# Kernel tuning notes

Measured on AMD Instinct MI355X. Metric: run time of the kernel, lower is better.

The kernel has to match this reference:

```python
import jax, jax.numpy as jnp
import numpy as np

B, N, D, HID, NB, NC = 64, 256, 1024, 512, 2, 1000
EPS = 1e-5

def _ln(x, g, b):
    m = x.mean(-1, keepdims=True)
    v = ((x - m) ** 2).mean(-1, keepdims=True)
    return (x - m) / jnp.sqrt(v + EPS) * g + b

def _gelu(x):
    return jax.nn.gelu(x, approximate=False)

def _knn_adjacency(x, k):
    # x: [N, D] -> symmetric-normalized kNN adjacency with self loops, [N, N]
    n = x.shape[0]
    sq = jnp.sum(x * x, axis=-1)
    d2 = sq[:, None] + sq[None, :] - 2.0 * (x @ x.T)
    d2 = jnp.where(jnp.eye(n, dtype=bool), jnp.inf, d2)  # exclude self from kNN
    idx = jax.lax.top_k(-d2, k)[1]                       # [N, k] nearest neighbors
    A = jnp.zeros((n, n), x.dtype).at[jnp.arange(n)[:, None], idx].set(1.0)
    A = jnp.maximum(A, A.T) + jnp.eye(n, dtype=x.dtype)  # symmetrize + self loops
    dinv = jax.lax.rsqrt(A.sum(-1))                      # D^{-1/2}
    return A * dinv[:, None] * dinv[None, :]

def setup_inputs() -> dict:
    key = jax.random.key(0)
    ks = jax.random.split(key, 8)
    s = lambda i, shape: jax.random.normal(ks[i], shape, jnp.float32) * 0.02
    return {
        "tokens": jax.random.normal(ks[0], (B, N, D), jnp.float32),
        "W1": s(1, (NB, D, HID)), "b1": jnp.zeros((NB, HID), jnp.float32),
        "W2": s(2, (NB, HID, D)), "b2": jnp.zeros((NB, D), jnp.float32),
        "g1": jnp.ones((NB, D), jnp.float32), "be1": jnp.zeros((NB, D), jnp.float32),
        "g2": jnp.ones((NB, D), jnp.float32), "be2": jnp.zeros((NB, D), jnp.float32),
        "gr": jnp.ones((D,), jnp.float32), "br": jnp.zeros((D,), jnp.float32),
        "Wc": s(3, (D, NC)), "bc": jnp.zeros((NC,), jnp.float32),
        "k": 8,
    }

def reference(tokens, W1, b1, W2, b2, g1, be1, g2, be2, gr, br, Wc, bc, k):
    # tokens: [B, N, D] backbone features flattened to nodes (eval mode: dropout = identity)
    A = jax.vmap(lambda t: _knn_adjacency(t, k))(tokens)  # [B, N, N]
    x = tokens
    for i in range(NB):  # GraphBlock
        h = _ln(x, g1[i], be1[i])
        h = _gelu(jnp.einsum("bij,bjh->bih", A, h @ W1[i] + b1[i]))  # A_hat @ lin1
        h = jnp.einsum("bij,bjd->bid", A, h @ W2[i] + b2[i])          # A_hat @ lin2
        x = x + h
        x = x + _gelu(_ln(x, g2[i], be2[i]))
    x = _gelu(_ln(x, gr, br))      # readout
    out = x.mean(axis=1)           # graph mean-pool, [B, D]
    return out @ Wc + bc           # logits [B, NC]
```

## Files before the change

### kernel.cpp

```cpp
#include <hip/hip_runtime.h>
#include <hip/hip_bf16.h>
#include <math.h>

constexpr int Bb  = 64;
constexpr int Nn_ = 256;
constexpr int Dd  = 1024;
constexpr int Hh  = 512;
constexpr int NC  = 1000;
constexpr float LN_EPS = 1e-5f;

#define DEV __device__ __forceinline__

typedef unsigned short u16;
typedef __attribute__((ext_vector_type(8))) short bf16x8;
typedef __attribute__((ext_vector_type(4))) float f32x4;
typedef __attribute__((ext_vector_type(4))) unsigned short u16x4;

DEV float gelu_f(float x) { return 0.5f * x * (1.0f + erff(x * 0.70710678118654752f)); }
DEV u16 bfb(float x) { __hip_bfloat16 h = __float2bfloat16(x); u16 u; __builtin_memcpy(&u, &h, 2); return u; }
DEV float fromb(u16 u) { unsigned int w = (unsigned int)u << 16; float f; __builtin_memcpy(&f, &w, 4); return f; }

DEV void gload16(const void* g, void* l) {
    __builtin_amdgcn_global_load_lds(
        (const __attribute__((address_space(1))) void*)(uintptr_t)g,
        (__attribute__((address_space(3))) void*)(uintptr_t)l, 16, 0, 0);
}

enum { EP_BIAS_BF_CT = 0, EP_GELU_BF_CT = 1, EP_BF = 2, EP_SBIAS_ADD_F32 = 3 };

template<int EPI>
__global__ __launch_bounds__(256) void mgemm_k(
    const u16* __restrict__ Ag, const u16* __restrict__ Bg, void* __restrict__ Cg,
    const float* __restrict__ bias, const float* __restrict__ addsrc, const float* __restrict__ rsA,
    int M, int Nc, int K, long sA, long sB, long sC)
{
    __shared__ __align__(16) u16 sm[2][2][128 * 32];
    const int tid = threadIdx.x;
    const int l = tid & 63, w = tid >> 6;
    const int wm = w >> 1, wn = w & 1;
    const int bm = blockIdx.y * 128, bn = blockIdx.x * 128;
    const int z = blockIdx.z;
    const u16* Ab  = Ag + (long)z * sA;
    const u16* Bbp = Bg + (long)z * sB;

    f32x4 acc[4][4] = {};
    const int nt = K >> 5;

    auto stage = [&](int db, int t) {
        const long kk = (long)t << 5;
        #pragma unroll
        for (int i = 0; i < 2; ++i) {
            const int o = w * 1024 + i * 4096 + l * 16;
            const int r = o >> 6;
            const int g = ((o >> 4) & 3) ^ ((r >> 1) & 3);
            gload16(Ab  + (long)(bm + r) * K + kk + g * 8, (char*)&sm[db][0][0] + o);
            gload16(Bbp + (long)(bn + r) * K + kk + g * 8, (char*)&sm[db][1][0] + o);
        }
    };

    stage(0, 0);
    __syncthreads();
    for (int t = 0; t < nt; ++t) {
        const int db = t & 1;
        if (t + 1 < nt) stage(db ^ 1, t + 1);
        const int lr = l & 15, g = l >> 4;
        bf16x8 af[4], bfr[4];
        #pragma unroll
        for (int fm = 0; fm < 4; ++fm) {
            const int r = wm * 64 + fm * 16 + lr;
            af[fm] = *(const bf16x8*)((const char*)&sm[db][0][0] + r * 64 + ((g ^ ((r >> 1) & 3)) << 4));
        }
        #pragma unroll
        for (int fn = 0; fn < 4; ++fn) {
            const int r = wn * 64 + fn * 16 + lr;
            bfr[fn] = *(const bf16x8*)((const char*)&sm[db][1][0] + r * 64 + ((g ^ ((r >> 1) & 3)) << 4));
        }
        #pragma unroll
        for (int fm = 0; fm < 4; ++fm)
            #pragma unroll
            for (int fn = 0; fn < 4; ++fn)
                acc[fm][fn] = __builtin_amdgcn_mfma_f32_16x16x32_bf16(af[fm], bfr[fn], acc[fm][fn], 0, 0, 0);
        __syncthreads();
    }

    const int lr = l & 15, lg = l >> 4;
    if constexpr (EPI == EP_SBIAS_ADD_F32) {
        float* Cb = (float*)Cg;
        #pragma unroll
        for (int fm = 0; fm < 4; ++fm)
            #pragma unroll
            for (int fn = 0; fn < 4; ++fn) {
                const int gc = bn + wn * 64 + fn * 16 + lr;
                const float bv = bias[gc];
                #pragma unroll
                for (int rg = 0; rg < 4; ++rg) {
                    const int gm = bm + wm * 64 + fm * 16 + lg * 4 + rg;
                    Cb[(long)gm * Nc + gc] = acc[fm][fn][rg] + rsA[gm] * bv + addsrc[(long)gm * Nc + gc];
                }
            }
    } else if constexpr (EPI == EP_BIAS_BF_CT || EPI == EP_GELU_BF_CT) {
        #pragma unroll
        for (int fm = 0; fm < 4; ++fm) {
            const int gm0 = bm + wm * 64 + fm * 16 + lg * 4;
            #pragma unroll
            for (int fn = 0; fn < 4; ++fn) {
                const int gc = bn + wn * 64 + fn * 16 + lr;
                u16x4 vals;
                if constexpr (EPI == EP_BIAS_BF_CT) {
                    const float bv = bias[gc];
                    #pragma unroll
                    for (int rg = 0; rg < 4; ++rg) vals[rg] = bfb(acc[fm][fn][rg] + bv);
                } else {
                    #pragma unroll
                    for (int rg = 0; rg < 4; ++rg) vals[rg] = bfb(gelu_f(acc[fm][fn][rg]));
                }
                long addr;
                if constexpr (EPI == EP_BIAS_BF_CT)
                    addr = (long)(gm0 >> 8) * ((long)Nc * 256) + (long)gc * 256 + (gm0 & 255);
                else
                    addr = (long)z * sC + (long)gc * 256 + gm0;
                *(u16x4*)&((u16*)Cg)[addr] = vals;
            }
        }
    } else {
        u16* Cb = (u16*)Cg + (long)z * sC;
        #pragma unroll
        for (int fm = 0; fm < 4; ++fm)
            #pragma unroll
            for (int fn = 0; fn < 4; ++fn)
                #pragma unroll
                for (int rg = 0; rg < 4; ++rg) {
                    const int gm = bm + wm * 64 + fm * 16 + lg * 4 + rg;
                    const int gc = bn + wn * 64 + fn * 16 + lr;
                    Cb[(long)gm * Nc + gc] = bfb(acc[fm][fn][rg]);
                }
    }
}

__global__ __launch_bounds__(256) void d2mm_k(
    const u16* __restrict__ HL, const float* __restrict__ sq, float* __restrict__ d2)
{
    __shared__ __align__(16) u16 sm[2][4][128 * 32];
    const int tid = threadIdx.x;
    const int l = tid & 63, w = tid >> 6;
    const int wm = w >> 1, wn = w & 1;

    const int lid = blockIdx.x;
    const int xcd = lid & 7, q = lid >> 3;
    const int j   = q % 3;
    const int z   = (q / 3) * 8 + xcd;
    const int bm  = (j == 2) ? 128 : 0;
    const int bn  = (j == 0) ? 0 : 128;

    const u16* Hb = HL + (long)z * Nn_ * 2048;

    f32x4 acc[4][4] = {};

    auto stage = [&](int db, int t) {
        const long kk = (long)t << 5;
        #pragma unroll
        for (int i = 0; i < 2; ++i) {
            const int o = w * 1024 + i * 4096 + l * 16;
            const int r = o >> 6;
            const int g = ((o >> 4) & 3) ^ ((r >> 1) & 3);
            const long ka = kk + g * 8;
            gload16(Hb + (long)(bm + r) * 2048 + ka,        (char*)&sm[db][0][0] + o);
            gload16(Hb + (long)(bm + r) * 2048 + 1024 + ka, (char*)&sm[db][1][0] + o);
            gload16(Hb + (long)(bn + r) * 2048 + ka,        (char*)&sm[db][2][0] + o);
            gload16(Hb + (long)(bn + r) * 2048 + 1024 + ka, (char*)&sm[db][3][0] + o);
        }
    };

    stage(0, 0);
    __syncthreads();
    for (int t = 0; t < 32; ++t) {
        const int db = t & 1;
        if (t + 1 < 32) stage(db ^ 1, t + 1);
        const int lr = l & 15, g = l >> 4;
        bf16x8 ah[4], al[4], bh[4], bl[4];
        #pragma unroll
        for (int fm = 0; fm < 4; ++fm) {
            const int r = wm * 64 + fm * 16 + lr;
            const int off = r * 64 + ((g ^ ((r >> 1) & 3)) << 4);
            ah[fm] = *(const bf16x8*)((const char*)&sm[db][0][0] + off);
            al[fm] = *(const bf16x8*)((const char*)&sm[db][1][0] + off);
        }
        #pragma unroll
        for (int fn = 0; fn < 4; ++fn) {
            const int r = wn * 64 + fn * 16 + lr;
            const int off = r * 64 + ((g ^ ((r >> 1) & 3)) << 4);
            bh[fn] = *(const bf16x8*)((const char*)&sm[db][2][0] + off);
            bl[fn] = *(const bf16x8*)((const char*)&sm[db][3][0] + off);
        }
        #pragma unroll
        for (int fm = 0; fm < 4; ++fm)
            #pragma unroll
            for (int fn = 0; fn < 4; ++fn) {
                acc[fm][fn] = __builtin_amdgcn_mfma_f32_16x16x32_bf16(ah[fm], bh[fn], acc[fm][fn], 0, 0, 0);
                acc[fm][fn] = __builtin_amdgcn_mfma_f32_16x16x32_bf16(ah[fm], bl[fn], acc[fm][fn], 0, 0, 0);
                acc[fm][fn] = __builtin_amdgcn_mfma_f32_16x16x32_bf16(al[fm], bh[fn], acc[fm][fn], 0, 0, 0);
            }
        __syncthreads();
    }

    const int lr = l & 15, lg = l >> 4;
    const float* sqb = sq + z * Nn_;
    float* ob = d2 + (long)z * Nn_ * Nn_;
    #pragma unroll
    for (int fm = 0; fm < 4; ++fm)
        #pragma unroll
        for (int fn = 0; fn < 4; ++fn)
            #pragma unroll
            for (int rg = 0; rg < 4; ++rg) {
                const int gm = bm + wm * 64 + fm * 16 + lg * 4 + rg;
                const int gc = bn + wn * 64 + fn * 16 + lr;
                float v = sqb[gm] + sqb[gc] - 2.0f * acc[fm][fn][rg];
                if (gm == gc) v = INFINITY;
                ob[(long)gm * Nn_ + gc] = v;
                if (j == 1) ob[(long)gc * Nn_ + gm] = v;
            }
}

__global__ __launch_bounds__(256) void prep_k(const float* __restrict__ in, u16* __restrict__ hilo,
    float* __restrict__ sq, u16* __restrict__ lnout,
    const float* __restrict__ g, const float* __restrict__ bvec)
{
    const long row = blockIdx.x;
    const int t = threadIdx.x;
    const float4 v = *(const float4*)&in[row * Dd + t * 4];
    float xs[4] = {v.x, v.y, v.z, v.w};

    u16x4 hi, lo;
    #pragma unroll
    for (int j = 0; j < 4; ++j) {
        hi[j] = bfb(xs[j]);
        lo[j] = bfb(xs[j] - fromb(hi[j]));
    }
    *(u16x4*)&hilo[row * 2048 + t * 4]        = hi;
    *(u16x4*)&hilo[row * 2048 + 1024 + t * 4] = lo;

    float s  = xs[0] + xs[1] + xs[2] + xs[3];
    float s2 = xs[0]*xs[0] + xs[1]*xs[1] + xs[2]*xs[2] + xs[3]*xs[3];
    #pragma unroll
    for (int o = 32; o > 0; o >>= 1) { s += __shfl_down(s, o); s2 += __shfl_down(s2, o); }
    __shared__ float sh[8];
    const int wid = t >> 6, lane = t & 63;
    if (lane == 0) { sh[wid] = s; sh[4 + wid] = s2; }
    __syncthreads();
    const float S  = sh[0] + sh[1] + sh[2] + sh[3];
    const float S2 = sh[4] + sh[5] + sh[6] + sh[7];
    if (t == 0) sq[row] = S2;
    const float mean = S * (1.0f / Dd);
    const float rstd = rsqrtf(S2 * (1.0f / Dd) - mean * mean + LN_EPS);
    const float4 gv = *(const float4*)&g[t * 4];
    const float4 bv = *(const float4*)&bvec[t * 4];
    const float gs[4] = {gv.x, gv.y, gv.z, gv.w};
    const float bs[4] = {bv.x, bv.y, bv.z, bv.w};
    u16x4 ov;
    #pragma unroll
    for (int j = 0; j < 4; ++j) ov[j] = bfb((xs[j] - mean) * rstd * gs[j] + bs[j]);
    *(u16x4*)&lnout[row * Dd + t * 4] = ov;
}

__global__ __launch_bounds__(256) void transw_k(const float* __restrict__ in, u16* __restrict__ out,
                                                int R, int C, long sIn, long sOut)
{
    __shared__ u16 t[32][33];
    const int z = blockIdx.z;
    const float* ib = in + (long)z * sIn;
    u16* ob = out + (long)z * sOut;
    const int r0 = blockIdx.y * 32, c0 = blockIdx.x * 32;
    const int tr = threadIdx.x >> 3, tc4 = (threadIdx.x & 7) * 4;
    const float* p = ib + (long)(r0 + tr) * C + c0 + tc4;
    #pragma unroll
    for (int j = 0; j < 4; ++j) t[tr][tc4 + j] = bfb(p[j]);
    __syncthreads();
    u16* q = ob + (long)(c0 + tr) * R + r0 + tc4;
    #pragma unroll
    for (int j = 0; j < 4; ++j) q[j] = t[tc4 + j][tr];
}

__global__ __launch_bounds__(256) void transc_k(const float* __restrict__ Wc, float* __restrict__ WcT)
{
    __shared__ float t[32][33];
    const int r0 = blockIdx.y * 32, c0 = blockIdx.x * 32;
    const int tr = threadIdx.x >> 3, tc4 = (threadIdx.x & 7) * 4;
    #pragma unroll
    for (int j = 0; j < 4; ++j) {
        const int c = c0 + tc4 + j;
        t[tr][tc4 + j] = (c < NC) ? Wc[(long)(r0 + tr) * NC + c] : 0.f;
    }
    __syncthreads();
    const int oc = c0 + tr;
    if (oc < NC) {
        #pragma unroll
        for (int j = 0; j < 4; ++j)
            WcT[(long)oc * Dd + r0 + tc4 + j] = t[tc4 + j][tr];
    }
}

template<int LAST>
__global__ __launch_bounds__(256) void ln2f_k(const float* __restrict__ xin,
    float* __restrict__ xout, u16* __restrict__ lnout,
    const float* __restrict__ g2, const float* __restrict__ be2,
    const float* __restrict__ gn, const float* __restrict__ bn)
{
    const long row = blockIdx.x;
    const int t = threadIdx.x;
    const int wid = t >> 6, lane = t & 63;
    __shared__ float sh[8];

    float4 v = *(const float4*)&xin[row * Dd + t * 4];
    float xs[4] = {v.x, v.y, v.z, v.w};
    float s = xs[0] + xs[1] + xs[2] + xs[3];
    float s2 = xs[0]*xs[0] + xs[1]*xs[1] + xs[2]*xs[2] + xs[3]*xs[3];
    #pragma unroll
    for (int o = 32; o > 0; o >>= 1) { s += __shfl_down(s, o); s2 += __shfl_down(s2, o); }
    if (lane == 0) { sh[wid] = s; sh[4 + wid] = s2; }
    __syncthreads();
    {
        const float S = sh[0] + sh[1] + sh[2] + sh[3];
        const float S2 = sh[4] + sh[5] + sh[6] + sh[7];
        const float mean = S * (1.0f / Dd);
        const float rstd = rsqrtf(S2 * (1.0f / Dd) - mean * mean + LN_EPS);
        const float4 gv = *(const float4*)&g2[t * 4];
        const float4 bv = *(const float4*)&be2[t * 4];
        const float gs[4] = {gv.x, gv.y, gv.z, gv.w};
        const float bs[4] = {bv.x, bv.y, bv.z, bv.w};
        #pragma unroll
        for (int j = 0; j < 4; ++j)
            xs[j] = xs[j] + gelu_f((xs[j] - mean) * rstd * gs[j] + bs[j]);
    }
    __syncthreads();
    float t1 = xs[0] + xs[1] + xs[2] + xs[3];
    float t2 = xs[0]*xs[0] + xs[1]*xs[1] + xs[2]*xs[2] + xs[3]*xs[3];
    #pragma unroll
    for (int o = 32; o > 0; o >>= 1) { t1 += __shfl_down(t1, o); t2 += __shfl_down(t2, o); }
    if (lane == 0) { sh[wid] = t1; sh[4 + wid] = t2; }
    __syncthreads();
    const float S = sh[0] + sh[1] + sh[2] + sh[3];
    const float S2 = sh[4] + sh[5] + sh[6] + sh[7];
    const float mean = S * (1.0f / Dd);
    const float rstd = rsqrtf(S2 * (1.0f / Dd) - mean * mean + LN_EPS);
    const float4 gv = *(const float4*)&gn[t * 4];
    const float4 bv = *(const float4*)&bn[t * 4];
    const float gs[4] = {gv.x, gv.y, gv.z, gv.w};
    const float bs[4] = {bv.x, bv.y, bv.z, bv.w};
    u16x4 ov;
    if constexpr (LAST) {
        #pragma unroll
        for (int j = 0; j < 4; ++j) ov[j] = bfb(gelu_f((xs[j] - mean) * rstd * gs[j] + bs[j]));
    } else {
        *(float4*)&xout[row * Dd + t * 4] = make_float4(xs[0], xs[1], xs[2], xs[3]);
        #pragma unroll
        for (int j = 0; j < 4; ++j) ov[j] = bfb((xs[j] - mean) * rstd * gs[j] + bs[j]);
    }
    *(u16x4*)&lnout[row * Dd + t * 4] = ov;
}

__global__ __launch_bounds__(256) void topk_k(const float* __restrict__ d2, float* __restrict__ Aout,
                                              const int* __restrict__ kptr)
{
    const int k = *kptr;
    const int wid = threadIdx.x >> 6, lane = threadIdx.x & 63;
    const long row = (long)blockIdx.x * 4 + wid;
    const long b = row >> 8;
    const int  i = (int)(row & 255);
    const float* dr = d2 + row * Nn_;
    float v[4];
    bool sel[4] = {false, false, false, false};
    #pragma unroll
    for (int c = 0; c < 4; ++c) v[c] = dr[lane + 64 * c];
    for (int it = 0; it < k; ++it) {
        float bv = INFINITY; int bi = 1 << 20;
        #pragma unroll
        for (int c = 0; c < 4; ++c) {
            const int idx = lane + 64 * c;
            if (!sel[c] && (v[c] < bv || (v[c] == bv && idx < bi))) { bv = v[c]; bi = idx; }
        }
        #pragma unroll
        for (int o = 32; o > 0; o >>= 1) {
            float ov = __shfl_xor(bv, o); int oi = __shfl_xor(bi, o);
            if (ov < bv || (ov == bv && oi < bi)) { bv = ov; bi = oi; }
        }
        #pragma unroll
        for (int c = 0; c < 4; ++c) if (lane + 64 * c == bi) sel[c] = true;
        if (lane == 0) {
            Aout[(b * Nn_ + i) * Nn_ + bi] = 1.0f;
            Aout[(b * Nn_ + bi) * Nn_ + i] = 1.0f;
        }
    }
    if (lane == 0) Aout[(b * Nn_ + i) * Nn_ + i] = 1.0f;
}

__global__ __launch_bounds__(256) void deg_k(const float* __restrict__ A, float* __restrict__ dinv)
{
    const int wid = threadIdx.x >> 6, lane = threadIdx.x & 63;
    const long row = (long)blockIdx.x * 4 + wid;
    const float* ar = A + row * Nn_;
    float s = 0.f;
    #pragma unroll
    for (int c = 0; c < 4; ++c) s += ar[lane + 64 * c];
    #pragma unroll
    for (int o = 32; o > 0; o >>= 1) s += __shfl_down(s, o);
    if (lane == 0) dinv[row] = rsqrtf(s);
}

__global__ __launch_bounds__(256) void scalebf2_k(const float* __restrict__ A, const float* __restrict__ dinv,
                                                  u16* __restrict__ out, float* __restrict__ rsA)
{
    const int wid = threadIdx.x >> 6, lane = threadIdx.x & 63;
    const long row = (long)blockIdx.x * 4 + wid;
    const long b = row >> 8;
    const float di = dinv[row];
    const int j0 = lane * 4;
    const float4 dj = *(const float4*)&dinv[b * Nn_ + j0];
    const float4 a = *(const float4*)&A[row * Nn_ + j0];
    const float v0 = a.x * di * dj.x, v1 = a.y * di * dj.y, v2 = a.z * di * dj.z, v3 = a.w * di * dj.w;
    u16x4 o = { bfb(v0), bfb(v1), bfb(v2), bfb(v3) };
    *(u16x4*)&out[row * Nn_ + j0] = o;
    float s = v0 + v1 + v2 + v3;
    #pragma unroll
    for (int off = 32; off > 0; off >>= 1) s += __shfl_down(s, off);
    if (lane == 0) rsA[row] = s;
}

__global__ __launch_bounds__(256) void poolb_k(const u16* __restrict__ y, float* __restrict__ pooled)
{
    const int d = blockIdx.x * 256 + threadIdx.x;
    const int b = blockIdx.y;
    const u16* yb = y + (long)b * Nn_ * Dd + d;
    float s = 0.f;
    #pragma unroll 4
    for (int n = 0; n < Nn_; ++n) s += fromb(yb[(long)n * Dd]);
    pooled[b * Dd + d] = s * (1.0f / Nn_);
}

__global__ __launch_bounds__(256) void cls2_k(const float* __restrict__ pooled, const float* __restrict__ WcT,
    const float* __restrict__ bc, float* __restrict__ out)
{
    const int w = threadIdx.x >> 6, lane = threadIdx.x & 63;
    const int c = blockIdx.x * 4 + w;
    const int b = blockIdx.y;
    const float* wr = WcT + (long)c * Dd;
    const float* p  = pooled + (long)b * Dd;
    float s = 0.f;
    #pragma unroll
    for (int it = 0; it < 4; ++it) {
        const float4 wv = *(const float4*)&wr[it * 256 + lane * 4];
        const float4 pv = *(const float4*)&p[it * 256 + lane * 4];
        s += wv.x * pv.x + wv.y * pv.y + wv.z * pv.z + wv.w * pv.w;
    }
    #pragma unroll
    for (int o = 32; o > 0; o >>= 1) s += __shfl_down(s, o);
    if (lane == 0) out[(long)b * NC + c] = s + bc[c];
}

extern "C" void kernel_launch(void* const* d_in, const int* in_sizes, int n_in,
                              void* d_out, int out_size, void* d_ws, size_t ws_size,
                              hipStream_t stream)
{
    const float* tokens = (const float*)d_in[0];
    const float* W1  = (const float*)d_in[1];
    const float* b1  = (const float*)d_in[2];
    const float* W2  = (const float*)d_in[3];
    const float* b2  = (const float*)d_in[4];
    const float* g1  = (const float*)d_in[5];
    const float* be1 = (const float*)d_in[6];
    const float* g2  = (const float*)d_in[7];
    const float* be2 = (const float*)d_in[8];
    const float* gr  = (const float*)d_in[9];
    const float* br  = (const float*)d_in[10];
    const float* Wc  = (const float*)d_in[11];
    const float* bc  = (const float*)d_in[12];
    const int*   kptr = (const int*)d_in[13];

    constexpr long SZ_XD = (long)Bb * Nn_ * Dd;
    constexpr long SZ_A  = (long)Bb * Nn_ * Nn_;

    char* wp = (char*)d_ws;
    float* x      = (float*)wp; wp += SZ_XD * 4;
    u16*   bufA   = (u16*)wp;   wp += SZ_XD * 2;
    u16*   bufB   = (u16*)wp;   wp += SZ_XD * 2;
    u16*   bufC   = (u16*)wp;   wp += SZ_XD * 2;
    u16*   AmatBF = (u16*)wp;   wp += SZ_A * 2;
    u16*   W1t    = (u16*)wp;   wp += 2L * Dd * Hh * 2;
    u16*   W2t    = (u16*)wp;   wp += 2L * Hh * Dd * 2;
    float* WcT    = (float*)wp; wp += (long)NC * Dd * 4;
    float* sq     = (float*)wp; wp += (long)Bb * Nn_ * 4;
    float* dinv   = (float*)wp; wp += (long)Bb * Nn_ * 4;
    float* rsA    = (float*)wp; wp += (long)Bb * Nn_ * 4;
    float* pooled = (float*)wp; wp += (long)Bb * Dd * 4;

    u16*   hilo  = bufA;
    float* d2f   = x;
    float* AmatF = x + SZ_A;
    u16*   robuf = bufA;

    const dim3 blk(256);

    prep_k<<<Bb * Nn_, blk, 0, stream>>>(tokens, hilo, sq, bufC, g1, be1);

    d2mm_k<<<192, blk, 0, stream>>>(hilo, sq, d2f);
    hipMemsetAsync(AmatF, 0, SZ_A * sizeof(float), stream);
    topk_k<<<Bb * Nn_ / 4, blk, 0, stream>>>(d2f, AmatF, kptr);
    deg_k<<<Bb * Nn_ / 4, blk, 0, stream>>>(AmatF, dinv);
    scalebf2_k<<<Bb * Nn_ / 4, blk, 0, stream>>>(AmatF, dinv, AmatBF, rsA);

    transw_k<<<dim3(Hh / 32, Dd / 32, 2), blk, 0, stream>>>(W1, W1t, Dd, Hh, (long)Dd * Hh, (long)Hh * Dd);
    transw_k<<<dim3(Dd / 32, Hh / 32, 2), blk, 0, stream>>>(W2, W2t, Hh, Dd, (long)Hh * Dd, (long)Dd * Hh);
    transc_k<<<dim3(32, Dd / 32), blk, 0, stream>>>(Wc, WcT);

    for (int i = 0; i < 2; ++i) {
        const float* xin = (i == 0) ? tokens : x;
        mgemm_k<EP_BIAS_BF_CT><<<dim3(Hh / 128, Bb * Nn_ / 128, 1), blk, 0, stream>>>(
            bufC, W1t + (long)i * Hh * Dd, bufB, b1 + i * Hh, nullptr, nullptr,
            Bb * Nn_, Hh, Dd, 0, 0, 0);
        mgemm_k<EP_GELU_BF_CT><<<dim3(Hh / 128, Nn_ / 128, Bb), blk, 0, stream>>>(
            AmatBF, bufB, bufA, nullptr, nullptr, nullptr,
            Nn_, Hh, Nn_, (long)Nn_ * Nn_, (long)Hh * Nn_, (long)Hh * Nn_);
        mgemm_k<EP_BF><<<dim3(Hh / 128, Nn_ / 128, Bb), blk, 0, stream>>>(
            AmatBF, bufA, bufB, nullptr, nullptr, nullptr,
            Nn_, Hh, Nn_, (long)Nn_ * Nn_, (long)Hh * Nn_, (long)Nn_ * Hh);
        mgemm_k<EP_SBIAS_ADD_F32><<<dim3(Dd / 128, Bb * Nn_ / 128, 1), blk, 0, stream>>>(
            bufB, W2t + (long)i * Dd * Hh, x, b2 + i * Dd, xin, rsA,
            Bb * Nn_, Dd, Hh, 0, 0, 0);
        if (i == 0)
            ln2f_k<0><<<Bb * Nn_, blk, 0, stream>>>(x, x, bufC, g2, be2, g1 + Dd, be1 + Dd);
        else
            ln2f_k<1><<<Bb * Nn_, blk, 0, stream>>>(x, nullptr, robuf, g2 + Dd, be2 + Dd, gr, br);
    }

    poolb_k<<<dim3(Dd / 256, Bb), blk, 0, stream>>>(robuf, pooled);
    cls2_k<<<dim3(NC / 4, Bb), blk, 0, stream>>>(pooled, WcT, bc, (float*)d_out);
}
```

Baseline: 429.7 us.

## Move residual add into LN kernel and store residual stream in bf16

The lin2 GEMM epilogue no longer reads the fp32 residual and writes fp32 x. It now writes only a bf16 h buffer. The LN2 kernel reads h plus the residual (fp32 tokens in block 0, bf16 x in block 1), does the add, and stores the updated residual as bf16. This cuts the GEMM epilogue's global traffic and halves the size of the residual buffer, at the cost of lower precision for the residual stream between blocks.

```diff
diff --git a/kernel.cpp b/kernel.cpp
--- a/kernel.cpp
+++ b/kernel.cpp
@@ -26,12 +26,12 @@
         (__attribute__((address_space(3))) void*)(uintptr_t)l, 16, 0, 0);
 }
 
-enum { EP_BIAS_BF_CT = 0, EP_GELU_BF_CT = 1, EP_BF = 2, EP_SBIAS_ADD_F32 = 3 };
+enum { EP_BIAS_BF_CT = 0, EP_GELU_BF_CT = 1, EP_BF = 2, EP_SBIAS_BF = 3 };
 
 template<int EPI>
 __global__ __launch_bounds__(256) void mgemm_k(
     const u16* __restrict__ Ag, const u16* __restrict__ Bg, void* __restrict__ Cg,
-    const float* __restrict__ bias, const float* __restrict__ addsrc, const float* __restrict__ rsA,
+    const float* __restrict__ bias, const float* __restrict__ rsA,
     int M, int Nc, int K, long sA, long sB, long sC)
 {
     __shared__ __align__(16) u16 sm[2][2][128 * 32];
@@ -84,8 +84,8 @@
     }
 
     const int lr = l & 15, lg = l >> 4;
-    if constexpr (EPI == EP_SBIAS_ADD_F32) {
-        float* Cb = (float*)Cg;
+    if constexpr (EPI == EP_SBIAS_BF) {
+        u16* Cb = (u16*)Cg;
         #pragma unroll
         for (int fm = 0; fm < 4; ++fm)
             #pragma unroll
@@ -95,7 +95,7 @@
                 #pragma unroll
                 for (int rg = 0; rg < 4; ++rg) {
                     const int gm = bm + wm * 64 + fm * 16 + lg * 4 + rg;
-                    Cb[(long)gm * Nc + gc] = acc[fm][fn][rg] + rsA[gm] * bv + addsrc[(long)gm * Nc + gc];
+                    Cb[(long)gm * Nc + gc] = bfb(acc[fm][fn][rg] + rsA[gm] * bv);
                 }
             }
     } else if constexpr (EPI == EP_BIAS_BF_CT || EPI == EP_GELU_BF_CT) {
@@ -299,9 +299,9 @@
     }
 }
 
-template<int LAST>
-__global__ __launch_bounds__(256) void ln2f_k(const float* __restrict__ xin,
-    float* __restrict__ xout, u16* __restrict__ lnout,
+template<int LAST, int XF32>
+__global__ __launch_bounds__(256) void ln2fr_k(const u16* __restrict__ hsrc,
+    const void* __restrict__ xinv, u16* __restrict__ xout, u16* __restrict__ lnout,
     const float* __restrict__ g2, const float* __restrict__ be2,
     const float* __restrict__ gn, const float* __restrict__ bn)
 {
@@ -310,8 +310,19 @@
     const int wid = t >> 6, lane = t & 63;
     __shared__ float sh[8];
 
-    float4 v = *(const float4*)&xin[row * Dd + t * 4];
-    float xs[4] = {v.x, v.y, v.z, v.w};
+    const u16x4 hv = *(const u16x4*)&hsrc[row * Dd + t * 4];
+    float xs[4];
+    if constexpr (XF32) {
+        const float4 xv = *(const float4*)&((const float*)xinv)[row * Dd + t * 4];
+        xs[0] = xv.x; xs[1] = xv.y; xs[2] = xv.z; xs[3] = xv.w;
+    } else {
+        const u16x4 xv = *(const u16x4*)&((const u16*)xinv)[row * Dd + t * 4];
+        #pragma unroll
+        for (int j = 0; j < 4; ++j) xs[j] = fromb(xv[j]);
+    }
+    #pragma unroll
+    for (int j = 0; j < 4; ++j) xs[j] += fromb(hv[j]);
+
     float s = xs[0] + xs[1] + xs[2] + xs[3];
     float s2 = xs[0]*xs[0] + xs[1]*xs[1] + xs[2]*xs[2] + xs[3]*xs[3];
     #pragma unroll
@@ -351,7 +362,10 @@
         #pragma unroll
         for (int j = 0; j < 4; ++j) ov[j] = bfb(gelu_f((xs[j] - mean) * rstd * gs[j] + bs[j]));
     } else {
-        *(float4*)&xout[row * Dd + t * 4] = make_float4(xs[0], xs[1], xs[2], xs[3]);
+        u16x4 xo;
+        #pragma unroll
+        for (int j = 0; j < 4; ++j) xo[j] = bfb(xs[j]);
+        *(u16x4*)&xout[row * Dd + t * 4] = xo;
         #pragma unroll
         for (int j = 0; j < 4; ++j) ov[j] = bfb((xs[j] - mean) * rstd * gs[j] + bs[j]);
     }
@@ -479,7 +493,8 @@
     constexpr long SZ_A  = (long)Bb * Nn_ * Nn_;
 
     char* wp = (char*)d_ws;
-    float* x      = (float*)wp; wp += SZ_XD * 4;
+    u16*   xbf    = (u16*)wp;   wp += SZ_XD * 2;
+    u16*   hbuf   = (u16*)wp;   wp += SZ_XD * 2;
     u16*   bufA   = (u16*)wp;   wp += SZ_XD * 2;
     u16*   bufB   = (u16*)wp;   wp += SZ_XD * 2;
     u16*   bufC   = (u16*)wp;   wp += SZ_XD * 2;
@@ -493,8 +508,8 @@
     float* pooled = (float*)wp; wp += (long)Bb * Dd * 4;
 
     u16*   hilo  = bufA;
-    float* d2f   = x;
-    float* AmatF = x + SZ_A;
+    float* d2f   = (float*)hbuf;
+    float* AmatF = (float*)xbf;
     u16*   robuf = bufA;
 
     const dim3 blk(256);
@@ -512,23 +527,24 @@
     transc_k<<<dim3(32, Dd / 32), blk, 0, stream>>>(Wc, WcT);
 
     for (int i = 0; i < 2; ++i) {
-        const float* xin = (i == 0) ? tokens : x;
         mgemm_k<EP_BIAS_BF_CT><<<dim3(Hh / 128, Bb * Nn_ / 128, 1), blk, 0, stream>>>(
-            bufC, W1t + (long)i * Hh * Dd, bufB, b1 + i * Hh, nullptr, nullptr,
+            bufC, W1t + (long)i * Hh * Dd, bufB, b1 + i * Hh, nullptr,
             Bb * Nn_, Hh, Dd, 0, 0, 0);
         mgemm_k<EP_GELU_BF_CT><<<dim3(Hh / 128, Nn_ / 128, Bb), blk, 0, stream>>>(
-            AmatBF, bufB, bufA, nullptr, nullptr, nullptr,
+            AmatBF, bufB, bufA, nullptr, nullptr,
             Nn_, Hh, Nn_, (long)Nn_ * Nn_, (long)Hh * Nn_, (long)Hh * Nn_);
         mgemm_k<EP_BF><<<dim3(Hh / 128, Nn_ / 128, Bb), blk, 0, stream>>>(
-            AmatBF, bufA, bufB, nullptr, nullptr, nullptr,
+            AmatBF, bufA, bufB, nullptr, nullptr,
             Nn_, Hh, Nn_, (long)Nn_ * Nn_, (long)Hh * Nn_, (long)Nn_ * Hh);
-        mgemm_k<EP_SBIAS_ADD_F32><<<dim3(Dd / 128, Bb * Nn_ / 128, 1), blk, 0, stream>>>(
-            bufB, W2t + (long)i * Dd * Hh, x, b2 + i * Dd, xin, rsA,
+        mgemm_k<EP_SBIAS_BF><<<dim3(Dd / 128, Bb * Nn_ / 128, 1), blk, 0, stream>>>(
+            bufB, W2t + (long)i * Dd * Hh, hbuf, b2 + i * Dd, rsA,
             Bb * Nn_, Dd, Hh, 0, 0, 0);
         if (i == 0)
-            ln2f_k<0><<<Bb * Nn_, blk, 0, stream>>>(x, x, bufC, g2, be2, g1 + Dd, be1 + Dd);
+            ln2fr_k<0, 1><<<Bb * Nn_, blk, 0, stream>>>(hbuf, tokens, xbf, bufC,
+                g2, be2, g1 + Dd, be1 + Dd);
         else
-            ln2f_k<1><<<Bb * Nn_, blk, 0, stream>>>(x, nullptr, robuf, g2 + Dd, be2 + Dd, gr, br);
+            ln2fr_k<1, 0><<<Bb * Nn_, blk, 0, stream>>>(hbuf, xbf, nullptr, robuf,
+                g2 + Dd, be2 + Dd, gr, br);
     }
 
     poolb_k<<<dim3(Dd / 256, Bb), blk, 0, stream>>>(robuf, pooled);
```

New measurement: 408.7 us. -4.9%, faster.
